# Kernel tuning notes

Hardware: AMD Instinct MI355X
Metric: run time of the kernel (lower is better)

Reference implementation:

```python
import jax, jax.numpy as jnp
import numpy as np

B, H, L, D = 8, 8, 2048, 64
FACTOR = 5


def _num_sel(length):
    return min(int(FACTOR * np.ceil(np.log(length))), length)


def setup_inputs() -> dict:
    key = jax.random.key(0)
    kq, kk, kv, ki = jax.random.split(key, 4)
    num_k = _num_sel(L)
    return {
        "q": jax.random.normal(kq, (B, H, L, D), dtype=jnp.float32),
        "k": jax.random.normal(kk, (B, H, L, D), dtype=jnp.float32),
        "v": jax.random.normal(kv, (B, H, L, D), dtype=jnp.float32),
        "random_index": jax.random.randint(ki, (L, num_k), 0, L, dtype=jnp.int32),
    }


def reference(q, k, v, random_index):
    b, h, q_len, d = q.shape
    k_len = k.shape[2]
    num_q = _num_sel(q_len)

    # --- random K sampling per query: k_s[b,h,i,j,:] = k[b,h,random_index[i,j],:]
    k_s = k[:, :, random_index, :]                      # (B,H,L,num_k,D)
    pre_attn = jnp.einsum('bhid,bhijd->bhij', q, k_s)   # (B,H,L,num_k)
    measure = pre_attn.max(-1) - pre_attn.sum(-1) / k_len  # (B,H,L)

    # --- top-k query selection (sorted=False in torch; order-insensitive math)
    _, idx = jax.lax.top_k(measure, num_q)              # (B,H,num_q)
    q_sel = jnp.take_along_axis(q, idx[..., None], axis=2)  # (B,H,num_q,D)

    # --- reduced attention over all keys
    attn = jnp.einsum('bhid,bhjd->bhij', q_sel, k) * (d ** -0.5)  # (B,H,num_q,k_len)

    # ProbMask: causal mask per selected query index (mask where j > idx[i])
    mask = jnp.arange(k_len)[None, None, None, :] > idx[..., None]
    attn = jnp.where(mask, -jnp.inf, attn)
    attn = jax.nn.softmax(attn, axis=-1)

    out_sel = jnp.einsum('bhij,bhjd->bhid', attn, v)    # (B,H,num_q,D)

    # --- context initialization (use_mask=True branch) and scatter back
    context = jnp.cumsum(v, axis=2)                     # (B,H,L,D)
    bi = jnp.arange(b)[:, None, None]
    hi = jnp.arange(h)[None, :, None]
    out = context.at[bi, hi, idx].set(out_sel)          # (B,H,L,D)
    return out, attn
```

## Files before the change

kernel.cpp:

```cpp
#include <hip/hip_runtime.h>
#include <float.h>
#include <math.h>

#define B_  8
#define H_  8
#define L_  2048
#define D_  64
#define NS  40
#define BH  (B_*H_)
#define SCALE 0.125f

__global__ __launch_bounds__(256) void measure_kernel(
    const float* __restrict__ q, const float* __restrict__ k,
    const int* __restrict__ ridx, float* __restrict__ measure)
{
    int wave = threadIdx.x >> 6, lane = threadIdx.x & 63;
    int qid = blockIdx.x * 4 + wave;
    int bh  = qid >> 11;
    int i   = qid & (L_ - 1);
    int g   = lane >> 2;
    int sl  = lane & 3;

    const float4* kb = (const float4*)(k + (size_t)bh * L_ * D_);
    const float4* qp = (const float4*)(q + ((size_t)bh * L_ + i) * D_);

    float4 q0 = qp[sl], q1 = qp[4 + sl], q2 = qp[8 + sl], q3 = qp[12 + sl];

    float mx = -FLT_MAX, sm = 0.f;
    #pragma unroll
    for (int p = 0; p < 3; ++p) {
        int s = p * 16 + g;
        bool valid = (s < NS);
        int r = ridx[i * NS + (valid ? s : NS - 1)];
        const float4* kr = kb + (size_t)r * 16;
        float4 k0 = kr[sl], k1 = kr[4 + sl], k2 = kr[8 + sl], k3 = kr[12 + sl];
        float pp = q0.x*k0.x + q0.y*k0.y + q0.z*k0.z + q0.w*k0.w
                 + q1.x*k1.x + q1.y*k1.y + q1.z*k1.z + q1.w*k1.w
                 + q2.x*k2.x + q2.y*k2.y + q2.z*k2.z + q2.w*k2.w
                 + q3.x*k3.x + q3.y*k3.y + q3.z*k3.z + q3.w*k3.w;
        pp += __shfl_xor(pp, 1, 64);
        pp += __shfl_xor(pp, 2, 64);
        if (valid) { mx = fmaxf(mx, pp); sm += pp; }
    }
    #pragma unroll
    for (int off = 4; off < 64; off <<= 1) {
        mx = fmaxf(mx, __shfl_xor(mx, off, 64));
        sm += __shfl_xor(sm, off, 64);
    }
    if (lane == 0)
        measure[(size_t)bh * L_ + i] = mx - sm * (1.0f / (float)L_);
}

__global__ __launch_bounds__(256) void topk_kernel(
    const float* __restrict__ measure, int* __restrict__ idxOut)
{
    __shared__ float wv[4]; __shared__ int wi[4];
    __shared__ float bvS;   __shared__ int biS;
    int bh = blockIdx.x, t = threadIdx.x;
    const float4* m4 = (const float4*)(measure + (size_t)bh * L_);
    float vals[8];
    float4 a = m4[t*2], b = m4[t*2 + 1];
    vals[0]=a.x; vals[1]=a.y; vals[2]=a.z; vals[3]=a.w;
    vals[4]=b.x; vals[5]=b.y; vals[6]=b.z; vals[7]=b.w;

    float lv = -FLT_MAX; int li = t*8;
    #pragma unroll
    for (int e = 0; e < 8; ++e) if (vals[e] > lv) { lv = vals[e]; li = t*8 + e; }

    int lane = t & 63, w = t >> 6;
    for (int r = 0; r < NS; ++r) {
        float v = lv; int idx = li;
        #pragma unroll
        for (int off = 32; off; off >>= 1) {
            float ov = __shfl_xor(v, off, 64);
            int   oi = __shfl_xor(idx, off, 64);
            if (ov > v || (ov == v && oi < idx)) { v = ov; idx = oi; }
        }
        if (lane == 0) { wv[w] = v; wi[w] = idx; }
        __syncthreads();
        if (t == 0) {
            float bv = wv[0]; int bi = wi[0];
            #pragma unroll
            for (int ww = 1; ww < 4; ++ww)
                if (wv[ww] > bv || (wv[ww] == bv && wi[ww] < bi)) { bv = wv[ww]; bi = wi[ww]; }
            bvS = bv; biS = bi;
            idxOut[bh * NS + r] = bi;
        }
        __syncthreads();
        int bi = biS;
        if ((bi >> 3) == t) {
            #pragma unroll
            for (int e = 0; e < 8; ++e) if ((bi & 7) == e) vals[e] = -FLT_MAX;
            lv = -FLT_MAX; li = t*8;
            #pragma unroll
            for (int e = 0; e < 8; ++e) if (vals[e] > lv) { lv = vals[e]; li = t*8 + e; }
        }
        __syncthreads();
    }
}

__global__ __launch_bounds__(256) void cumsum_p1(
    const float* __restrict__ v, float4* __restrict__ vpart)
{
    __shared__ float4 part[16][16];
    int bh = blockIdx.x >> 4, c = blockIdx.x & 15;
    int d4 = threadIdx.x & 15, sub = threadIdx.x >> 4;
    const float4* vb = (const float4*)(v + (size_t)bh * L_ * D_);
    int r0 = c*128 + sub*8;
    float4 s = make_float4(0,0,0,0);
    #pragma unroll
    for (int r = 0; r < 8; ++r) {
        float4 x = vb[(r0 + r)*16 + d4];
        s.x += x.x; s.y += x.y; s.z += x.z; s.w += x.w;
    }
    part[sub][d4] = s;
    __syncthreads();
    if (sub == 0) {
        float4 tot = part[0][d4];
        #pragma unroll
        for (int ss = 1; ss < 16; ++ss) {
            float4 x = part[ss][d4];
            tot.x += x.x; tot.y += x.y; tot.z += x.z; tot.w += x.w;
        }
        vpart[(bh*16 + c)*16 + d4] = tot;
    }
}

__global__ __launch_bounds__(256) void cumsum_p2(
    const float* __restrict__ v, const float4* __restrict__ vpart,
    float* __restrict__ out)
{
    __shared__ float4 part[16][16];
    int bh = blockIdx.x >> 4, c = blockIdx.x & 15;
    int d4 = threadIdx.x & 15, sub = threadIdx.x >> 4;
    const float4* vb = (const float4*)(v + (size_t)bh * L_ * D_);
    float4*       ob = (float4*)(out + (size_t)bh * L_ * D_);
    int r0 = c*128 + sub*8;
    float4 s = make_float4(0,0,0,0);
    #pragma unroll
    for (int r = 0; r < 8; ++r) {
        float4 x = vb[(r0 + r)*16 + d4];
        s.x += x.x; s.y += x.y; s.z += x.z; s.w += x.w;
    }
    part[sub][d4] = s;
    float4 run = make_float4(0,0,0,0);
    for (int cc = 0; cc < c; ++cc) {
        float4 x = vpart[(bh*16 + cc)*16 + d4];
        run.x += x.x; run.y += x.y; run.z += x.z; run.w += x.w;
    }
    __syncthreads();
    #pragma unroll
    for (int ss = 0; ss < 16; ++ss) {
        if (ss < sub) {
            float4 x = part[ss][d4];
            run.x += x.x; run.y += x.y; run.z += x.z; run.w += x.w;
        }
    }
    #pragma unroll
    for (int r = 0; r < 8; ++r) {
        float4 x = vb[(r0 + r)*16 + d4];
        run.x += x.x; run.y += x.y; run.z += x.z; run.w += x.w;
        ob[(r0 + r)*16 + d4] = run;
    }
}

__global__ __launch_bounds__(256) void scores_kernel(
    const float* __restrict__ q, const float* __restrict__ k,
    const int* __restrict__ idxSel, float* __restrict__ attn)
{
    __shared__ float4 kbuf[16 * 129];
    int bh = blockIdx.x / 10, grp = blockIdx.x % 10;
    int qi = threadIdx.x >> 6, sub = threadIdx.x & 63;
    int rank = grp*4 + qi;
    int qrow = idxSel[bh*NS + rank];

    const float4* qrp = (const float4*)(q + ((size_t)bh * L_ + qrow) * D_);
    float4 qreg[16];
    #pragma unroll
    for (int g = 0; g < 16; ++g) qreg[g] = qrp[g];

    const float4* kb = (const float4*)(k + (size_t)bh * L_ * D_);
    float sc0[16], sc1[16];

    #pragma unroll
    for (int c = 0; c < 16; ++c) {
        __syncthreads();
        int j0 = c * 128;
        #pragma unroll
        for (int it = 0; it < 8; ++it) {
            int fi = threadIdx.x + 256*it;
            int g = fi & 15, j = fi >> 4;
            kbuf[g*129 + j] = kb[(size_t)(j0 + j)*16 + g];
        }
        __syncthreads();
        float acc0 = 0.f, acc1 = 0.f;
        #pragma unroll
        for (int g = 0; g < 16; ++g) {
            float4 k0 = kbuf[g*129 + sub];
            float4 k1 = kbuf[g*129 + sub + 64];
            float4 qq = qreg[g];
            acc0 += qq.x*k0.x + qq.y*k0.y + qq.z*k0.z + qq.w*k0.w;
            acc1 += qq.x*k1.x + qq.y*k1.y + qq.z*k1.z + qq.w*k1.w;
        }
        sc0[c] = acc0 * SCALE;
        sc1[c] = acc1 * SCALE;
    }

    float mx = -FLT_MAX;
    #pragma unroll
    for (int c = 0; c < 16; ++c) {
        if (c*128 + sub      <= qrow) mx = fmaxf(mx, sc0[c]);
        if (c*128 + sub + 64 <= qrow) mx = fmaxf(mx, sc1[c]);
    }
    #pragma unroll
    for (int off = 32; off; off >>= 1) mx = fmaxf(mx, __shfl_xor(mx, off, 64));

    float sum = 0.f;
    #pragma unroll
    for (int c = 0; c < 16; ++c) {
        sc0[c] = (c*128 + sub      <= qrow) ? __expf(sc0[c] - mx) : 0.f;
        sc1[c] = (c*128 + sub + 64 <= qrow) ? __expf(sc1[c] - mx) : 0.f;
        sum += sc0[c] + sc1[c];
    }
    #pragma unroll
    for (int off = 32; off; off >>= 1) sum += __shfl_xor(sum, off, 64);
    float inv = 1.f / sum;

    float* arow = attn + (size_t)(bh*NS + rank) * L_;
    #pragma unroll
    for (int c = 0; c < 16; ++c) {
        arow[c*128 + sub]      = sc0[c] * inv;
        arow[c*128 + sub + 64] = sc1[c] * inv;
    }
}

__global__ __launch_bounds__(256) void pv_kernel(
    const float* __restrict__ v, const int* __restrict__ idxSel,
    const float* __restrict__ attn, float* __restrict__ out)
{
    __shared__ float wl[4][L_ + 64];
    __shared__ float4 part[16][16];
    __shared__ int qr4[4];
    int bh = blockIdx.x / 10, grp = blockIdx.x % 10;
    int t = threadIdx.x;
    if (t < 4) qr4[t] = idxSel[bh*NS + grp*4 + t];

    #pragma unroll
    for (int it = 0; it < 8; ++it) {
        int f = t + 256*it;
        int rr = f >> 9, fi = f & 511;
        const float4* ar = (const float4*)(attn + (size_t)(bh*NS + grp*4 + rr) * L_);
        float4 x = ar[fi];
        int j = 4*fi;
        *((float4*)&wl[rr][j + 4*(j >> 7)]) = x;
    }
    __syncthreads();

    int maxq = max(max(qr4[0], qr4[1]), max(qr4[2], qr4[3]));
    int d4 = t & 15, seg = t >> 4;
    const float4* vb = (const float4*)(v + (size_t)bh * L_ * D_);
    float4 acc[4];
    #pragma unroll
    for (int rr = 0; rr < 4; ++rr) acc[rr] = make_float4(0,0,0,0);

    int jlo = seg*128, jhi = min(jlo + 127, maxq);
    for (int j = jlo; j <= jhi; ++j) {
        float4 x = vb[(size_t)j*16 + d4];
        int jp = j + 4*(j >> 7);
        #pragma unroll
        for (int rr = 0; rr < 4; ++rr) {
            float wgt = wl[rr][jp];
            acc[rr].x += wgt*x.x; acc[rr].y += wgt*x.y;
            acc[rr].z += wgt*x.z; acc[rr].w += wgt*x.w;
        }
    }

    #pragma unroll
    for (int rr = 0; rr < 4; ++rr) {
        part[seg][d4] = acc[rr];
        __syncthreads();
        float4 a = acc[rr];
        for (int s2 = 8; s2; s2 >>= 1) {
            if (seg < s2) {
                float4 o = part[seg + s2][d4];
                a.x += o.x; a.y += o.y; a.z += o.z; a.w += o.w;
                part[seg][d4] = a;
            }
            __syncthreads();
        }
        if (seg == 0) {
            float4* orow = (float4*)(out + ((size_t)bh * L_ + qr4[rr]) * D_);
            orow[d4] = a;
        }
        __syncthreads();
    }
}

extern "C" void kernel_launch(void* const* d_in, const int* in_sizes, int n_in,
                              void* d_out, int out_size, void* d_ws, size_t ws_size,
                              hipStream_t stream) {
    const float* q    = (const float*)d_in[0];
    const float* k    = (const float*)d_in[1];
    const float* v    = (const float*)d_in[2];
    const int*   ridx = (const int*)d_in[3];

    float* out     = (float*)d_out;
    float* attnOut = out + (size_t)BH * L_ * D_;

    float*  measure = (float*)d_ws;
    int*    idxSel  = (int*)((char*)d_ws + (size_t)BH * L_ * sizeof(float));
    float4* vpart   = (float4*)d_ws;

    measure_kernel<<<BH * L_ / 4, 256, 0, stream>>>(q, k, ridx, measure);
    topk_kernel   <<<BH,          256, 0, stream>>>(measure, idxSel);
    cumsum_p1     <<<BH * 16,     256, 0, stream>>>(v, vpart);
    cumsum_p2     <<<BH * 16,     256, 0, stream>>>(v, vpart, out);
    scores_kernel <<<BH * 10,     256, 0, stream>>>(q, k, idxSel, attnOut);
    pv_kernel     <<<BH * 10,     256, 0, stream>>>(v, idxSel, attnOut, out);
}
```

Before: 389.6 us.

## Remap block indices so each head stays on one XCD; rework measure gather

Each kernel's block index is remapped so that blocks belonging to the same (batch, head) slice land on the same XCD under round-robin dispatch. The aim is to keep that head's K/V rows local to one XCD's L2. The measure kernel is also restructured: the 40 random indices are loaded once per wave and broadcast by shuffle, and each lane handles one float4 of D across 10 passes of 4 samples, with no invalid-slot masking. This adds shuffle reductions and relies on the dispatcher assigning blocks to XCDs round-robin.

```diff
diff --git a/kernel.cpp b/kernel.cpp
--- a/kernel.cpp
+++ b/kernel.cpp
@@ -10,43 +10,40 @@
 #define BH  (B_*H_)
 #define SCALE 0.125f
 
+
 __global__ __launch_bounds__(256) void measure_kernel(
     const float* __restrict__ q, const float* __restrict__ k,
     const int* __restrict__ ridx, float* __restrict__ measure)
 {
     int wave = threadIdx.x >> 6, lane = threadIdx.x & 63;
-    int qid = blockIdx.x * 4 + wave;
-    int bh  = qid >> 11;
-    int i   = qid & (L_ - 1);
-    int g   = lane >> 2;
-    int sl  = lane & 3;
+    int b = blockIdx.x;
+    int xcd = b & 7, s = b >> 3;
+    int bh  = xcd + ((s >> 9) << 3);
+    int i   = (s & 511) * 4 + wave;
+    int qj  = lane >> 4;
+    int d4  = lane & 15;
+
+    int rs = ridx[i * NS + (lane < NS ? lane : NS - 1)];
 
     const float4* kb = (const float4*)(k + (size_t)bh * L_ * D_);
-    const float4* qp = (const float4*)(q + ((size_t)bh * L_ + i) * D_);
-
-    float4 q0 = qp[sl], q1 = qp[4 + sl], q2 = qp[8 + sl], q3 = qp[12 + sl];
+    float4 qq = ((const float4*)(q + ((size_t)bh * L_ + i) * D_))[d4];
 
     float mx = -FLT_MAX, sm = 0.f;
     #pragma unroll
-    for (int p = 0; p < 3; ++p) {
-        int s = p * 16 + g;
-        bool valid = (s < NS);
-        int r = ridx[i * NS + (valid ? s : NS - 1)];
-        const float4* kr = kb + (size_t)r * 16;
-        float4 k0 = kr[sl], k1 = kr[4 + sl], k2 = kr[8 + sl], k3 = kr[12 + sl];
-        float pp = q0.x*k0.x + q0.y*k0.y + q0.z*k0.z + q0.w*k0.w
-                 + q1.x*k1.x + q1.y*k1.y + q1.z*k1.z + q1.w*k1.w
-                 + q2.x*k2.x + q2.y*k2.y + q2.z*k2.z + q2.w*k2.w
-                 + q3.x*k3.x + q3.y*k3.y + q3.z*k3.z + q3.w*k3.w;
+    for (int p = 0; p < 10; ++p) {
+        int j = p * 4 + qj;
+        int r = __shfl(rs, j, 64);
+        float4 kk = kb[(size_t)r * 16 + d4];
+        float pp = qq.x*kk.x + qq.y*kk.y + qq.z*kk.z + qq.w*kk.w;
         pp += __shfl_xor(pp, 1, 64);
         pp += __shfl_xor(pp, 2, 64);
-        if (valid) { mx = fmaxf(mx, pp); sm += pp; }
-    }
-    #pragma unroll
-    for (int off = 4; off < 64; off <<= 1) {
-        mx = fmaxf(mx, __shfl_xor(mx, off, 64));
-        sm += __shfl_xor(sm, off, 64);
-    }
+        pp += __shfl_xor(pp, 4, 64);
+        pp += __shfl_xor(pp, 8, 64);
+        mx = fmaxf(mx, pp);
+        sm += pp;
+    }
+    mx = fmaxf(mx, __shfl_xor(mx, 16, 64));  sm += __shfl_xor(sm, 16, 64);
+    mx = fmaxf(mx, __shfl_xor(mx, 32, 64));  sm += __shfl_xor(sm, 32, 64);
     if (lane == 0)
         measure[(size_t)bh * L_ + i] = mx - sm * (1.0f / (float)L_);
 }
@@ -56,12 +53,14 @@
 {
     __shared__ float wv[4]; __shared__ int wi[4];
     __shared__ float bvS;   __shared__ int biS;
-    int bh = blockIdx.x, t = threadIdx.x;
+    int b = blockIdx.x;
+    int bh = (b & 7) + ((b >> 3) << 3);
+    int t = threadIdx.x;
     const float4* m4 = (const float4*)(measure + (size_t)bh * L_);
     float vals[8];
-    float4 a = m4[t*2], b = m4[t*2 + 1];
+    float4 a = m4[t*2], bb = m4[t*2 + 1];
     vals[0]=a.x; vals[1]=a.y; vals[2]=a.z; vals[3]=a.w;
-    vals[4]=b.x; vals[5]=b.y; vals[6]=b.z; vals[7]=b.w;
+    vals[4]=bb.x; vals[5]=bb.y; vals[6]=bb.z; vals[7]=bb.w;
 
     float lv = -FLT_MAX; int li = t*8;
     #pragma unroll
@@ -103,17 +102,20 @@
     const float* __restrict__ v, float4* __restrict__ vpart)
 {
     __shared__ float4 part[16][16];
-    int bh = blockIdx.x >> 4, c = blockIdx.x & 15;
+    int b = blockIdx.x;
+    int xcd = b & 7, s = b >> 3;
+    int bh = xcd + ((s >> 4) << 3);
+    int c  = s & 15;
     int d4 = threadIdx.x & 15, sub = threadIdx.x >> 4;
     const float4* vb = (const float4*)(v + (size_t)bh * L_ * D_);
     int r0 = c*128 + sub*8;
-    float4 s = make_float4(0,0,0,0);
+    float4 acc = make_float4(0,0,0,0);
     #pragma unroll
     for (int r = 0; r < 8; ++r) {
         float4 x = vb[(r0 + r)*16 + d4];
-        s.x += x.x; s.y += x.y; s.z += x.z; s.w += x.w;
-    }
-    part[sub][d4] = s;
+        acc.x += x.x; acc.y += x.y; acc.z += x.z; acc.w += x.w;
+    }
+    part[sub][d4] = acc;
     __syncthreads();
     if (sub == 0) {
         float4 tot = part[0][d4];
@@ -131,18 +133,21 @@
     float* __restrict__ out)
 {
     __shared__ float4 part[16][16];
-    int bh = blockIdx.x >> 4, c = blockIdx.x & 15;
+    int b = blockIdx.x;
+    int xcd = b & 7, s = b >> 3;
+    int bh = xcd + ((s >> 4) << 3);
+    int c  = s & 15;
     int d4 = threadIdx.x & 15, sub = threadIdx.x >> 4;
     const float4* vb = (const float4*)(v + (size_t)bh * L_ * D_);
     float4*       ob = (float4*)(out + (size_t)bh * L_ * D_);
     int r0 = c*128 + sub*8;
-    float4 s = make_float4(0,0,0,0);
+    float4 acc = make_float4(0,0,0,0);
     #pragma unroll
     for (int r = 0; r < 8; ++r) {
         float4 x = vb[(r0 + r)*16 + d4];
-        s.x += x.x; s.y += x.y; s.z += x.z; s.w += x.w;
-    }
-    part[sub][d4] = s;
+        acc.x += x.x; acc.y += x.y; acc.z += x.z; acc.w += x.w;
+    }
+    part[sub][d4] = acc;
     float4 run = make_float4(0,0,0,0);
     for (int cc = 0; cc < c; ++cc) {
         float4 x = vpart[(bh*16 + cc)*16 + d4];
@@ -169,7 +174,10 @@
     const int* __restrict__ idxSel, float* __restrict__ attn)
 {
     __shared__ float4 kbuf[16 * 129];
-    int bh = blockIdx.x / 10, grp = blockIdx.x % 10;
+    int b = blockIdx.x;
+    int xcd = b & 7, s = b >> 3;
+    int bh  = xcd + ((s / 10) << 3);
+    int grp = s % 10;
     int qi = threadIdx.x >> 6, sub = threadIdx.x & 63;
     int rank = grp*4 + qi;
     int qrow = idxSel[bh*NS + rank];
@@ -241,7 +249,10 @@
     __shared__ float wl[4][L_ + 64];
     __shared__ float4 part[16][16];
     __shared__ int qr4[4];
-    int bh = blockIdx.x / 10, grp = blockIdx.x % 10;
+    int b = blockIdx.x;
+    int xcd = b & 7, s = b >> 3;
+    int bh  = xcd + ((s / 10) << 3);
+    int grp = s % 10;
     int t = threadIdx.x;
     if (t < 4) qr4[t] = idxSel[bh*NS + grp*4 + t];
 
```

Measured after the change: 331.2 us. 1.18x faster.
